# Kernel tuning notes

Hardware: AMD Instinct MI355X
Metric: run time of the kernel (lower is better)

## Reference

```python
import jax, jax.numpy as jnp
import numpy as np

D = 2048
MAX_SEQ_LEN = 8192
LN_EPS = 1e-5


def _spine(max_len):
    s = [0, 2, 4]
    while True:
        nv = 2 * (s[-1] + s[-2] + s[-3])
        if nv >= max_len:
            break
        s.append(nv)
    return s


def setup_inputs() -> dict:
    key = jax.random.key(0)
    k0, k1 = jax.random.split(key, 2)
    B, S = 8, 8192
    x = jax.random.normal(k0, (B, S, D), dtype=jnp.float32)
    # LearnedHarmonicBasis params (torch init values)
    ones = jnp.ones((D,), jnp.float32)
    zeros = jnp.zeros((D,), jnp.float32)
    return {
        "x": x,
        "alpha_xz": ones, "beta_xy": -ones, "gamma_x": zeros,
        "alpha_wy": ones, "beta_wx": -ones, "gamma_w": zeros,
        "alpha_xv": ones, "beta_wv": -ones, "gamma_v": zeros,
        # nn.Linear(2D, D): weight [D, 2D], bias [D]
        "gate_w": (jax.random.normal(k1, (D, 2 * D), jnp.float32) / np.float32(np.sqrt(2 * D))),
        "gate_b": zeros,
        "ln_w": ones,
        "ln_b": zeros,
    }


def _layernorm(v, w, b):
    m = jnp.mean(v, axis=-1, keepdims=True)
    var = jnp.var(v, axis=-1, keepdims=True)
    return (v - m) * jax.lax.rsqrt(var + LN_EPS) * w + b


def reference(x, alpha_xz, beta_xy, gamma_x, alpha_wy, beta_wx, gamma_w,
              alpha_xv, beta_wv, gamma_v, gate_w, gate_b, ln_w, ln_b):
    S = x.shape[1]
    rel = [i for i in _spine(MAX_SEQ_LEN) if i < S]  # static at trace time
    h = x
    for k in range(3, len(rel)):  # strictly sequential spine recurrence
        pz, py, px = rel[k], rel[k - 1], rel[k - 2]
        z = h[:, pz, :]        # (B, D)
        y = h[:, py, :]
        x_prev = h[:, px, :]
        x_new = alpha_xz * z + beta_xy * y + gamma_x
        w = alpha_wy * y + beta_wx * x_prev + gamma_w
        v = alpha_xv * x_new + beta_wv * w + gamma_v
        # HierarchicalInjectionGate(v, z)
        g = jax.nn.sigmoid(jnp.concatenate([v, z], axis=-1) @ gate_w.T + gate_b)
        v_inj = _layernorm(g * v + (1.0 - g) * z, ln_w, ln_b)
        h = h.at[:, pz, :].set(v_inj)
    return h
```

## Files before the change

### kernel.cpp

```cpp
#include <hip/hip_runtime.h>

#define DD 2048
#define SS 8192
#define BB 8
#define TWO_D 4096
#define LN_EPS 1e-5f
#define NCHAIN 256
#define SLICE  9364
#define NCOPY  1171

typedef float f32x4 __attribute__((ext_vector_type(4)));

__device__ __forceinline__ bool is_spine(int r) {
    return (r==12)|(r==36)|(r==104)|(r==304)|(r==888)|(r==2592)|(r==7568);
}

__global__ __launch_bounds__(256) void k1f(
    int it, const float* __restrict__ x, int pz,
    const float* __restrict__ ybase, unsigned long long ybstr,
    const float* __restrict__ pbase, unsigned long long pbstr,
    const float* __restrict__ a_xz, const float* __restrict__ b_xy, const float* __restrict__ g_x,
    const float* __restrict__ a_wy, const float* __restrict__ b_wx, const float* __restrict__ g_w,
    const float* __restrict__ a_xv, const float* __restrict__ b_wv, const float* __restrict__ g_v,
    const float* __restrict__ gate_w, const float* __restrict__ gate_b,
    float* __restrict__ u_out, float* __restrict__ out)
{
    __shared__ float lds[BB][DD];
    const int tid = threadIdx.x, lane = tid & 63, wave = tid >> 6;
    const size_t bstr_x = (size_t)SS * DD;

    if (blockIdx.x >= NCHAIN) {
        const int cb = blockIdx.x - NCHAIN;
        const long long rbase = (long long)it * SLICE + (long long)cb * 8;
        const f32x4* src4 = (const f32x4*)x;
        f32x4* dst4 = (f32x4*)out;
        for (int rr = wave; rr < 8; rr += 4) {
            const long long row = rbase + rr;
            if (row >= (long long)BB * SS) continue;
            if (is_spine((int)(row & (SS - 1)))) continue;
            const f32x4* s = src4 + (size_t)row * 512;
            f32x4*       d = dst4 + (size_t)row * 512;
#pragma unroll
            for (int k = 0; k < 8; ++k)
                d[lane + 64 * k] = s[lane + 64 * k];
        }
        return;
    }

    const float* zrow = x + (size_t)pz * DD;

    for (int dd = 0; dd < DD; dd += 256) {
        const int d = dd + tid;
        const float axz = a_xz[d], bxy = b_xy[d], gx  = g_x[d];
        const float awy = a_wy[d], bwx = b_wx[d], gww = g_w[d];
        const float axv = a_xv[d], bwv = b_wv[d], gv  = g_v[d];
#pragma unroll
        for (int b = 0; b < BB; ++b) {
            const float z  = zrow[(size_t)b * bstr_x + d];
            const float y  = ybase[(size_t)b * ybstr + d];
            const float xp = pbase[(size_t)b * pbstr + d];
            lds[b][d] = axv * (axz * z + bxy * y + gx)
                      + bwv * (awy * y + bwx * xp + gww) + gv;
        }
    }
    __syncthreads();

    const int d0 = blockIdx.x * 8 + wave * 2;
    const int myb = lane & 7, myc = (lane >> 3) & 1;

    const float* gw0a = gate_w + (size_t)d0 * TWO_D;
    const float* gw1a = gw0a + TWO_D;
    float a0[8], a1[8];
#pragma unroll
    for (int b = 0; b < 8; ++b) { a0[b] = 0.f; a1[b] = 0.f; }
    for (int j = lane * 4; j < DD; j += 256) {
        const float4 w0 = *(const float4*)(gw0a + j);
        const float4 w1 = *(const float4*)(gw1a + j);
#pragma unroll
        for (int b = 0; b < 8; ++b) {
            const float4 vv = *(const float4*)&lds[b][j];
            a0[b] += w0.x*vv.x + w0.y*vv.y + w0.z*vv.z + w0.w*vv.w;
            a1[b] += w1.x*vv.x + w1.y*vv.y + w1.z*vv.z + w1.w*vv.w;
        }
    }
    const float vmine = (lane < 16) ? lds[myb][d0 + myc] : 0.f;
    __syncthreads();

    for (int d4 = tid; d4 < 512; d4 += 256) {
#pragma unroll
        for (int b = 0; b < BB; ++b)
            ((f32x4*)&lds[b][0])[d4] = ((const f32x4*)(zrow + (size_t)b * bstr_x))[d4];
    }
    __syncthreads();

    const float* gw0b = gw0a + DD;
    const float* gw1b = gw1a + DD;
    for (int j = lane * 4; j < DD; j += 256) {
        const float4 w0 = *(const float4*)(gw0b + j);
        const float4 w1 = *(const float4*)(gw1b + j);
#pragma unroll
        for (int b = 0; b < 8; ++b) {
            const float4 zz = *(const float4*)&lds[b][j];
            a0[b] += w0.x*zz.x + w0.y*zz.y + w0.z*zz.z + w0.w*zz.w;
            a1[b] += w1.x*zz.x + w1.y*zz.y + w1.z*zz.z + w1.w*zz.w;
        }
    }
#pragma unroll
    for (int b = 0; b < 8; ++b) {
#pragma unroll
        for (int off = 32; off >= 1; off >>= 1) {
            a0[b] += __shfl_xor(a0[b], off);
            a1[b] += __shfl_xor(a1[b], off);
        }
    }
    if (lane < 16) {
        const int d = d0 + myc;
        const float tot = myc ? a1[myb] : a0[myb];
        const float zmv = lds[myb][d];
        const float gg  = 1.f / (1.f + __expf(-(tot + gate_b[d])));
        u_out[myb * DD + d] = gg * vmine + (1.f - gg) * zmv;
    }
}

__global__ __launch_bounds__(256) void k2_ln(
    const float* __restrict__ u, const float* __restrict__ lnw,
    const float* __restrict__ lnb, float* __restrict__ dst,
    float* __restrict__ out, int pz)
{
    const int b = blockIdx.x, tid = threadIdx.x;
    const float* ub = u + b * DD;
    float vals[8];
    float s = 0.f, sq = 0.f;
#pragma unroll
    for (int i = 0; i < 8; ++i) {
        const float t = ub[tid + 256 * i];
        vals[i] = t; s += t; sq += t * t;
    }
    const int wave = tid >> 6, lane = tid & 63;
#pragma unroll
    for (int off = 32; off >= 1; off >>= 1) {
        s  += __shfl_xor(s, off);
        sq += __shfl_xor(sq, off);
    }
    __shared__ float red[2][4];
    if (lane == 0) { red[0][wave] = s; red[1][wave] = sq; }
    __syncthreads();
    s  = red[0][0] + red[0][1] + red[0][2] + red[0][3];
    sq = red[1][0] + red[1][1] + red[1][2] + red[1][3];
    const float mean = s * (1.f / DD);
    const float var  = sq * (1.f / DD) - mean * mean;
    const float rs   = rsqrtf(var + LN_EPS);
    float* db = dst + b * DD;
    float* ob = out + (size_t)b * SS * DD + (size_t)pz * DD;
#pragma unroll
    for (int i = 0; i < 8; ++i) {
        const int d = tid + 256 * i;
        const float r = (vals[i] - mean) * rs * lnw[d] + lnb[d];
        db[d] = r;
        ob[d] = r;
    }
}

extern "C" void kernel_launch(void* const* d_in, const int* in_sizes, int n_in,
                              void* d_out, int out_size, void* d_ws, size_t ws_size,
                              hipStream_t stream)
{
    const float* x      = (const float*)d_in[0];
    const float* a_xz   = (const float*)d_in[1];
    const float* b_xy   = (const float*)d_in[2];
    const float* g_x    = (const float*)d_in[3];
    const float* a_wy   = (const float*)d_in[4];
    const float* b_wx   = (const float*)d_in[5];
    const float* g_w    = (const float*)d_in[6];
    const float* a_xv   = (const float*)d_in[7];
    const float* b_wv   = (const float*)d_in[8];
    const float* g_v    = (const float*)d_in[9];
    const float* gate_w = (const float*)d_in[10];
    const float* gate_b = (const float*)d_in[11];
    const float* ln_w   = (const float*)d_in[12];
    const float* ln_b   = (const float*)d_in[13];
    float* out = (float*)d_out;

    float* u_buf = (float*)d_ws;
    float* res   = u_buf + BB * DD;

    static const int PZ[7] = {12, 36, 104, 304, 888, 2592, 7568};
    static const int PY[7] = {4, 12, 36, 104, 304, 888, 2592};
    static const int PX[7] = {2, 4, 12, 36, 104, 304, 888};

    for (int it = 0; it < 7; ++it) {
        const float* ybase; unsigned long long ybstr;
        const float* pbase; unsigned long long pbstr;
        if (it == 0) { ybase = x + (size_t)PY[0] * DD; ybstr = (size_t)SS * DD; }
        else         { ybase = res + (size_t)(it - 1) * BB * DD; ybstr = DD; }
        if (it <= 1) { pbase = x + (size_t)PX[it] * DD; pbstr = (size_t)SS * DD; }
        else         { pbase = res + (size_t)(it - 2) * BB * DD; pbstr = DD; }

        hipLaunchKernelGGL(k1f, dim3(NCHAIN + NCOPY), dim3(256), 0, stream,
                           it, x, PZ[it], ybase, ybstr, pbase, pbstr,
                           a_xz, b_xy, g_x, a_wy, b_wx, g_w, a_xv, b_wv, g_v,
                           gate_w, gate_b, u_buf, out);
        hipLaunchKernelGGL(k2_ln, dim3(BB), dim3(256), 0, stream,
                           u_buf, ln_w, ln_b, res + (size_t)it * BB * DD,
                           out, PZ[it]);
    }
}
```

Before: 295.0 us.

## Halve LDS footprint by processing batch rows in two halves of four

The fused gate kernel now stages only four batch rows in shared memory at a time (32 KB instead of 64 KB), looping twice over the v and z halves. The smaller footprint lets more blocks reside per CU, which matters because the same kernel also runs the bulk copy blocks. The cost is that gate_w rows are streamed twice as many times per block and there are extra barriers.

```diff
diff --git a/kernel.cpp b/kernel.cpp
--- a/kernel.cpp
+++ b/kernel.cpp
@@ -15,7 +15,7 @@
     return (r==12)|(r==36)|(r==104)|(r==304)|(r==888)|(r==2592)|(r==7568);
 }
 
-__global__ __launch_bounds__(256) void k1f(
+__global__ __launch_bounds__(256) void k1h(
     int it, const float* __restrict__ x, int pz,
     const float* __restrict__ ybase, unsigned long long ybstr,
     const float* __restrict__ pbase, unsigned long long pbstr,
@@ -25,7 +25,7 @@
     const float* __restrict__ gate_w, const float* __restrict__ gate_b,
     float* __restrict__ u_out, float* __restrict__ out)
 {
-    __shared__ float lds[BB][DD];
+    __shared__ float lds4[4][DD];
     const int tid = threadIdx.x, lane = tid & 63, wave = tid >> 6;
     const size_t bstr_x = (size_t)SS * DD;
 
@@ -48,63 +48,74 @@
     }
 
     const float* zrow = x + (size_t)pz * DD;
-
-    for (int dd = 0; dd < DD; dd += 256) {
-        const int d = dd + tid;
-        const float axz = a_xz[d], bxy = b_xy[d], gx  = g_x[d];
-        const float awy = a_wy[d], bwx = b_wx[d], gww = g_w[d];
-        const float axv = a_xv[d], bwv = b_wv[d], gv  = g_v[d];
-#pragma unroll
-        for (int b = 0; b < BB; ++b) {
-            const float z  = zrow[(size_t)b * bstr_x + d];
-            const float y  = ybase[(size_t)b * ybstr + d];
-            const float xp = pbase[(size_t)b * pbstr + d];
-            lds[b][d] = axv * (axz * z + bxy * y + gx)
-                      + bwv * (awy * y + bwx * xp + gww) + gv;
-        }
-    }
-    __syncthreads();
-
     const int d0 = blockIdx.x * 8 + wave * 2;
     const int myb = lane & 7, myc = (lane >> 3) & 1;
 
+    float a0[8], a1[8];
+#pragma unroll
+    for (int b = 0; b < 8; ++b) { a0[b] = 0.f; a1[b] = 0.f; }
+    float vmine = 0.f, zmine = 0.f;
+
     const float* gw0a = gate_w + (size_t)d0 * TWO_D;
     const float* gw1a = gw0a + TWO_D;
-    float a0[8], a1[8];
-#pragma unroll
-    for (int b = 0; b < 8; ++b) { a0[b] = 0.f; a1[b] = 0.f; }
-    for (int j = lane * 4; j < DD; j += 256) {
-        const float4 w0 = *(const float4*)(gw0a + j);
-        const float4 w1 = *(const float4*)(gw1a + j);
-#pragma unroll
-        for (int b = 0; b < 8; ++b) {
-            const float4 vv = *(const float4*)&lds[b][j];
-            a0[b] += w0.x*vv.x + w0.y*vv.y + w0.z*vv.z + w0.w*vv.w;
-            a1[b] += w1.x*vv.x + w1.y*vv.y + w1.z*vv.z + w1.w*vv.w;
-        }
-    }
-    const float vmine = (lane < 16) ? lds[myb][d0 + myc] : 0.f;
-    __syncthreads();
-
-    for (int d4 = tid; d4 < 512; d4 += 256) {
-#pragma unroll
-        for (int b = 0; b < BB; ++b)
-            ((f32x4*)&lds[b][0])[d4] = ((const f32x4*)(zrow + (size_t)b * bstr_x))[d4];
-    }
-    __syncthreads();
+
+    for (int half = 0; half < 2; ++half) {
+        for (int dd = 0; dd < DD; dd += 256) {
+            const int d = dd + tid;
+            const float axz = a_xz[d], bxy = b_xy[d], gx  = g_x[d];
+            const float awy = a_wy[d], bwx = b_wx[d], gww = g_w[d];
+            const float axv = a_xv[d], bwv = b_wv[d], gv  = g_v[d];
+#pragma unroll
+            for (int i = 0; i < 4; ++i) {
+                const int b = half * 4 + i;
+                const float z  = zrow[(size_t)b * bstr_x + d];
+                const float y  = ybase[(size_t)b * ybstr + d];
+                const float xp = pbase[(size_t)b * pbstr + d];
+                lds4[i][d] = axv * (axz * z + bxy * y + gx)
+                           + bwv * (awy * y + bwx * xp + gww) + gv;
+            }
+        }
+        __syncthreads();
+        for (int j = lane * 4; j < DD; j += 256) {
+            const float4 w0 = *(const float4*)(gw0a + j);
+            const float4 w1 = *(const float4*)(gw1a + j);
+#pragma unroll
+            for (int i = 0; i < 4; ++i) {
+                const int b = half * 4 + i;
+                const float4 vv = *(const float4*)&lds4[i][j];
+                a0[b] += w0.x*vv.x + w0.y*vv.y + w0.z*vv.z + w0.w*vv.w;
+                a1[b] += w1.x*vv.x + w1.y*vv.y + w1.z*vv.z + w1.w*vv.w;
+            }
+        }
+        if (lane < 16 && (myb >> 2) == half) vmine = lds4[myb & 3][d0 + myc];
+        __syncthreads();
+    }
 
     const float* gw0b = gw0a + DD;
     const float* gw1b = gw1a + DD;
-    for (int j = lane * 4; j < DD; j += 256) {
-        const float4 w0 = *(const float4*)(gw0b + j);
-        const float4 w1 = *(const float4*)(gw1b + j);
-#pragma unroll
-        for (int b = 0; b < 8; ++b) {
-            const float4 zz = *(const float4*)&lds[b][j];
-            a0[b] += w0.x*zz.x + w0.y*zz.y + w0.z*zz.z + w0.w*zz.w;
-            a1[b] += w1.x*zz.x + w1.y*zz.y + w1.z*zz.z + w1.w*zz.w;
-        }
-    }
+    for (int half = 0; half < 2; ++half) {
+        for (int d4 = tid; d4 < 512; d4 += 256) {
+#pragma unroll
+            for (int i = 0; i < 4; ++i)
+                ((f32x4*)&lds4[i][0])[d4] =
+                    ((const f32x4*)(zrow + (size_t)(half * 4 + i) * bstr_x))[d4];
+        }
+        __syncthreads();
+        for (int j = lane * 4; j < DD; j += 256) {
+            const float4 w0 = *(const float4*)(gw0b + j);
+            const float4 w1 = *(const float4*)(gw1b + j);
+#pragma unroll
+            for (int i = 0; i < 4; ++i) {
+                const int b = half * 4 + i;
+                const float4 zz = *(const float4*)&lds4[i][j];
+                a0[b] += w0.x*zz.x + w0.y*zz.y + w0.z*zz.z + w0.w*zz.w;
+                a1[b] += w1.x*zz.x + w1.y*zz.y + w1.z*zz.z + w1.w*zz.w;
+            }
+        }
+        if (lane < 16 && (myb >> 2) == half) zmine = lds4[myb & 3][d0 + myc];
+        __syncthreads();
+    }
+
 #pragma unroll
     for (int b = 0; b < 8; ++b) {
 #pragma unroll
@@ -116,9 +127,8 @@
     if (lane < 16) {
         const int d = d0 + myc;
         const float tot = myc ? a1[myb] : a0[myb];
-        const float zmv = lds[myb][d];
         const float gg  = 1.f / (1.f + __expf(-(tot + gate_b[d])));
-        u_out[myb * DD + d] = gg * vmine + (1.f - gg) * zmv;
+        u_out[myb * DD + d] = gg * vmine + (1.f - gg) * zmine;
     }
 }
 
@@ -196,7 +206,7 @@
         if (it <= 1) { pbase = x + (size_t)PX[it] * DD; pbstr = (size_t)SS * DD; }
         else         { pbase = res + (size_t)(it - 2) * BB * DD; pbstr = DD; }
 
-        hipLaunchKernelGGL(k1f, dim3(NCHAIN + NCOPY), dim3(256), 0, stream,
+        hipLaunchKernelGGL(k1h, dim3(NCHAIN + NCOPY), dim3(256), 0, stream,
                            it, x, PZ[it], ybase, ybstr, pbase, pbstr,
                            a_xz, b_xy, g_x, a_wy, b_wx, g_w, a_xv, b_wv, g_v,
                            gate_w, gate_b, u_buf, out);
```

Result: slower. 325.0 us (+10.2%).
